# Kernel optimization log

Measured on AMD Instinct MI355X. Metric: run time of the kernel, lower is better.

Reference implementation:

```python
import jax, jax.numpy as jnp
import numpy as np

NUM_USERS, NUM_ITEMS, D = 100000, 200000, 128
B, LLEN, SLEN = 4096, 200, 50
NEG = -1e9


def setup_inputs() -> dict:
    key = jax.random.key(0)
    ks = jax.random.split(key, 10)
    w_range = float(np.sqrt(3.0 / D))
    return {
        "user_table": 0.01 * jax.random.normal(ks[0], (NUM_USERS, D), dtype=jnp.float32),
        "item_table": 0.01 * jax.random.normal(ks[1], (NUM_ITEMS, D), dtype=jnp.float32),
        "W1": jax.random.uniform(ks[2], (2 * D, 16), minval=-w_range, maxval=w_range, dtype=jnp.float32),
        "b1": jnp.zeros((16,), dtype=jnp.float32),
        "W2": jax.random.uniform(ks[3], (16, 1), minval=-w_range, maxval=w_range, dtype=jnp.float32),
        "b2": jnp.zeros((1,), dtype=jnp.float32),
        "user_inputs": jax.random.randint(ks[4], (B,), 0, NUM_USERS, dtype=jnp.int64) if jax.config.jax_enable_x64 else jax.random.randint(ks[4], (B,), 0, NUM_USERS, dtype=jnp.int32),
        "L_inputs": jax.random.randint(ks[5], (B, LLEN), 0, NUM_ITEMS, dtype=jnp.int32),
        "S_inputs": jax.random.randint(ks[6], (B, SLEN), 0, NUM_ITEMS, dtype=jnp.int32),
        "item_inputs": jax.random.randint(ks[7], (B,), 0, NUM_ITEMS, dtype=jnp.int32),
    }


def reference(user_table, item_table, W1, b1, W2, b2,
              user_inputs, L_inputs, S_inputs, item_inputs):
    def att_logits(x):  # x: [..., 2D] -> [...]
        h = jax.nn.relu(x @ W1 + b1)
        return (h @ W2 + b2)[..., 0]

    def masked_softmax(logits, mask):  # softmax over last axis restricted to mask
        logits = jnp.where(mask, logits, NEG)
        return jax.nn.softmax(logits, axis=-1)

    u_emb = user_table[user_inputs]                      # [B, D]

    # ---- long-term attention over L history ----
    L_mask = L_inputs >= 0                               # [B, L]
    L_idx = jnp.where(L_mask, L_inputs, 0)
    L_emb = item_table[L_idx]                            # [B, L, D]
    uL = jnp.concatenate([jnp.broadcast_to(u_emb[:, None, :], L_emb.shape), L_emb], axis=-1)  # [B, L, 2D]
    w1 = masked_softmax(att_logits(uL), L_mask)          # [B, L]
    u_long = jnp.einsum('bl,bld->bd', w1, L_emb)         # [B, D]

    # ---- short-term attention over [u_long] + S (L assumed nonempty) ----
    S_mask = S_inputs >= 0                               # [B, S]
    S_idx = jnp.where(S_mask, S_inputs, 0)
    S_emb = item_table[S_idx]                            # [B, S, D]
    seq = jnp.concatenate([u_long[:, None, :], S_emb], axis=1)   # [B, 1+S, D]
    seq_mask = jnp.concatenate([jnp.ones((seq.shape[0], 1), dtype=bool), S_mask], axis=1)
    uSeq = jnp.concatenate([jnp.broadcast_to(u_emb[:, None, :], seq.shape), seq], axis=-1)  # [B, 1+S, 2D]
    w2 = masked_softmax(att_logits(uSeq), seq_mask)      # [B, 1+S]
    user_hybrid = jnp.einsum('bs,bsd->bd', w2, seq)      # [B, D]

    # ---- score: bmm([B,1,D], [B,D,1]) -> [B,1,1] ----
    item_emb = item_table[item_inputs]                   # [B, D]
    score = jnp.sum(user_hybrid * item_emb, axis=-1)[:, None, None]
    return score
```

## Files before the change

kernel.cpp:

```cpp
#include <hip/hip_runtime.h>
#include <math.h>

#define D 128
#define LLEN 200
#define SLEN 50
#define CH 56
#define ESTR 132

__device__ __forceinline__ float wave_red_sum(float v) {
#pragma unroll
  for (int m = 32; m >= 1; m >>= 1) v += __shfl_xor(v, m, 64);
  return v;
}
__device__ __forceinline__ float block_sum(float v, float* red) {
  v = wave_red_sum(v);
  if ((threadIdx.x & 63) == 0) red[threadIdx.x >> 6] = v;
  __syncthreads();
  v = red[0] + red[1] + red[2] + red[3];
  __syncthreads();
  return v;
}

#define GATHER_L(dst, IT, BASE)                        \
  do {                                                 \
    int s_ = tid + (IT);                               \
    int gid_ = rows1[(BASE) + (s_ >> 5)];              \
    if (gid_ < 0) gid_ = 0;                            \
    dst = it4[(size_t)gid_ * 32 + (s_ & 31)];          \
  } while (0)

#define GATHER_S(dst, IT)                              \
  do {                                                 \
    int s_ = tid + (IT);                               \
    int gid_ = rowsS[s_ >> 5];                         \
    if (gid_ < 0) gid_ = 0;                            \
    dst = it4[(size_t)gid_ * 32 + (s_ & 31)];          \
  } while (0)

#define STORE_L(src, IT)                                                     \
  do {                                                                       \
    int s_ = tid + (IT);                                                     \
    reinterpret_cast<float4*>(&ebuf[(s_ >> 5) * ESTR])[s_ & 31] = src;       \
  } while (0)

#define STORE_S(src, IT)                                                     \
  do {                                                                       \
    int s_ = tid + (IT);                                                     \
    reinterpret_cast<float4*>(&ebuf[((s_ >> 5) + 1) * ESTR])[s_ & 31] = src; \
  } while (0)

#define FMA4(WL, P, ACC)                \
  do {                                  \
    ACC.x = fmaf((WL), P.x, ACC.x);     \
    ACC.y = fmaf((WL), P.y, ACC.y);     \
    ACC.z = fmaf((WL), P.z, ACC.z);     \
  } while (0);                          \
  ACC.w = fmaf((WL), P.w, ACC.w)

#define MATVEC_HS(CNT)                                                      \
  if (lane < (CNT)) {                                                       \
    float a0 = 0.f, a1 = 0.f, a2 = 0.f, a3 = 0.f;                           \
    const float4* er4 = reinterpret_cast<const float4*>(&ebuf[lane * ESTR]);\
    const float* wc = &W1[(size_t)D * 16 + 4 * w];                          \
    _Pragma("unroll 8")                                                     \
    for (int k = 0; k < 32; ++k) {                                          \
      float4 e = er4[k];                                                    \
      const float* wr = wc + k * 64;            \
      a0 = fmaf(e.x, wr[0],  a0); a1 = fmaf(e.x, wr[1],  a1);               \
      a2 = fmaf(e.x, wr[2],  a2); a3 = fmaf(e.x, wr[3],  a3);               \
      a0 = fmaf(e.y, wr[16], a0); a1 = fmaf(e.y, wr[17], a1);               \
      a2 = fmaf(e.y, wr[18], a2); a3 = fmaf(e.y, wr[19], a3);               \
      a0 = fmaf(e.z, wr[32], a0); a1 = fmaf(e.z, wr[33], a1);               \
      a2 = fmaf(e.z, wr[34], a2); a3 = fmaf(e.z, wr[35], a3);               \
      a0 = fmaf(e.w, wr[48], a0); a1 = fmaf(e.w, wr[49], a1);               \
      a2 = fmaf(e.w, wr[50], a2); a3 = fmaf(e.w, wr[51], a3);               \
    }                                                                       \
    float hs = fmaxf(upart_sh[4 * w + 0] + a0, 0.f) * w2a;                  \
    hs = fmaf(fmaxf(upart_sh[4 * w + 1] + a1, 0.f), w2b, hs);               \
    hs = fmaf(fmaxf(upart_sh[4 * w + 2] + a2, 0.f), w2c, hs);               \
    hs = fmaf(fmaxf(upart_sh[4 * w + 3] + a3, 0.f), w2d, hs);               \
    hspart[w * 65 + lane] = hs;                                             \
  }

#define FINALIZE_L(CNT, BASE)                                           \
  if (tid < (CNT)) {                                                    \
    float lg = hspart[tid] + hspart[65 + tid] + hspart[130 + tid] +     \
               hspart[195 + tid] + b2v;                                 \
    float p_ = (rows1[(BASE) + tid] >= 0) ? expf(lg) : 0.f;             \
    w_sh[tid] = p_;                                                     \
    pacc += p_;                                                         \
  }

__global__ void __launch_bounds__(256, 5) din_kernel(
    const float* __restrict__ user_table, const float* __restrict__ item_table,
    const float* __restrict__ W1, const float* __restrict__ b1,
    const float* __restrict__ W2, const float* __restrict__ b2,
    const int* __restrict__ user_inputs, const int* __restrict__ L_inputs,
    const int* __restrict__ S_inputs, const int* __restrict__ item_inputs,
    float* __restrict__ out) {
  __shared__ float ebuf[CH * ESTR];
  __shared__ float hspart[4 * 65];
  __shared__ float w_sh[CH];
  __shared__ int rows1[LLEN];
  __shared__ int rowsS[SLEN];
  __shared__ float upart_sh[16];
  __shared__ float red_sh[4];

  const int b = blockIdx.x;
  const int tid = threadIdx.x;
  const int lane = tid & 63;
  const int w = __builtin_amdgcn_readfirstlane(tid >> 6);
  const int col4 = tid & 31;
  const int grp = tid >> 5;
  const float4* it4 = reinterpret_cast<const float4*>(item_table);

  float* u_sh = &ebuf[0];
  float* part = &ebuf[128];
  if (tid < D) u_sh[tid] = user_table[(size_t)user_inputs[b] * D + tid];
  const float item_f =
      (tid < D) ? item_table[(size_t)item_inputs[b] * D + tid] : 0.f;
  if (tid < LLEN) rows1[tid] = L_inputs[(size_t)b * LLEN + tid];
  if (tid < SLEN) rowsS[tid] = S_inputs[(size_t)b * SLEN + tid];
  __syncthreads();

  float4 A0, A1, A2, A3, A4, A5, A6, B0, B1, B2, B3, B4, B5, B6;
  GATHER_L(A0, 0, 0);    GATHER_L(A1, 256, 0);  GATHER_L(A2, 512, 0);
  GATHER_L(A3, 768, 0);  GATHER_L(A4, 1024, 0); GATHER_L(A5, 1280, 0);
  GATHER_L(A6, 1536, 0);

  {
    int j = tid & 15, g = tid >> 4;
    float p = 0.f;
#pragma unroll
    for (int t = 0; t < 8; ++t) {
      int d = g * 8 + t;
      p = fmaf(u_sh[d], W1[d * 16 + j], p);
    }
    part[tid] = p;
  }
  __syncthreads();
  if (tid < 16) {
    float s = b1[tid];
#pragma unroll
    for (int g = 0; g < 16; ++g) s += part[g * 16 + tid];
    upart_sh[tid] = s;
  }
  __syncthreads();

  const float b2v = b2[0];
  const float w2a = W2[4 * w + 0], w2b = W2[4 * w + 1];
  const float w2c = W2[4 * w + 2], w2d = W2[4 * w + 3];

  float pacc = 0.f;
  float4 uacc = make_float4(0.f, 0.f, 0.f, 0.f);
  float wl;

  STORE_L(A0, 0);    STORE_L(A1, 256);  STORE_L(A2, 512);  STORE_L(A3, 768);
  STORE_L(A4, 1024); STORE_L(A5, 1280); STORE_L(A6, 1536);
  __syncthreads();
  MATVEC_HS(56);
  GATHER_L(B0, 0, 56);    GATHER_L(B1, 256, 56);  GATHER_L(B2, 512, 56);
  GATHER_L(B3, 768, 56);  GATHER_L(B4, 1024, 56); GATHER_L(B5, 1280, 56);
  GATHER_L(B6, 1536, 56);
  __syncthreads();
  FINALIZE_L(56, 0);
  __syncthreads();
  wl = w_sh[grp];      FMA4(wl, A0, uacc);
  wl = w_sh[grp + 8];  FMA4(wl, A1, uacc);
  wl = w_sh[grp + 16]; FMA4(wl, A2, uacc);
  wl = w_sh[grp + 24]; FMA4(wl, A3, uacc);
  wl = w_sh[grp + 32]; FMA4(wl, A4, uacc);
  wl = w_sh[grp + 40]; FMA4(wl, A5, uacc);
  wl = w_sh[grp + 48]; FMA4(wl, A6, uacc);

  STORE_L(B0, 0);    STORE_L(B1, 256);  STORE_L(B2, 512);  STORE_L(B3, 768);
  STORE_L(B4, 1024); STORE_L(B5, 1280); STORE_L(B6, 1536);
  __syncthreads();
  MATVEC_HS(56);
  GATHER_L(A0, 0, 112);    GATHER_L(A1, 256, 112);  GATHER_L(A2, 512, 112);
  GATHER_L(A3, 768, 112);  GATHER_L(A4, 1024, 112); GATHER_L(A5, 1280, 112);
  GATHER_L(A6, 1536, 112);
  __syncthreads();
  FINALIZE_L(56, 56);
  __syncthreads();
  wl = w_sh[grp];      FMA4(wl, B0, uacc);
  wl = w_sh[grp + 8];  FMA4(wl, B1, uacc);
  wl = w_sh[grp + 16]; FMA4(wl, B2, uacc);
  wl = w_sh[grp + 24]; FMA4(wl, B3, uacc);
  wl = w_sh[grp + 32]; FMA4(wl, B4, uacc);
  wl = w_sh[grp + 40]; FMA4(wl, B5, uacc);
  wl = w_sh[grp + 48]; FMA4(wl, B6, uacc);

  STORE_L(A0, 0);    STORE_L(A1, 256);  STORE_L(A2, 512);  STORE_L(A3, 768);
  STORE_L(A4, 1024); STORE_L(A5, 1280); STORE_L(A6, 1536);
  __syncthreads();
  MATVEC_HS(56);
  GATHER_L(B0, 0, 168); GATHER_L(B1, 256, 168);
  GATHER_L(B2, 512, 168); GATHER_L(B3, 768, 168);
  __syncthreads();
  FINALIZE_L(56, 112);
  __syncthreads();
  wl = w_sh[grp];      FMA4(wl, A0, uacc);
  wl = w_sh[grp + 8];  FMA4(wl, A1, uacc);
  wl = w_sh[grp + 16]; FMA4(wl, A2, uacc);
  wl = w_sh[grp + 24]; FMA4(wl, A3, uacc);
  wl = w_sh[grp + 32]; FMA4(wl, A4, uacc);
  wl = w_sh[grp + 40]; FMA4(wl, A5, uacc);
  wl = w_sh[grp + 48]; FMA4(wl, A6, uacc);

  STORE_L(B0, 0); STORE_L(B1, 256); STORE_L(B2, 512); STORE_L(B3, 768);
  __syncthreads();
  MATVEC_HS(32);
  GATHER_S(A0, 0);    GATHER_S(A1, 256);  GATHER_S(A2, 512);
  GATHER_S(A3, 768);  GATHER_S(A4, 1024); GATHER_S(A5, 1280);
  if (tid < 64) GATHER_S(A6, 1536);
  __syncthreads();
  FINALIZE_L(32, 168);
  __syncthreads();
  wl = w_sh[grp];      FMA4(wl, B0, uacc);
  wl = w_sh[grp + 8];  FMA4(wl, B1, uacc);
  wl = w_sh[grp + 16]; FMA4(wl, B2, uacc);
  wl = w_sh[grp + 24]; FMA4(wl, B3, uacc);

  const float invS1 = 1.f / block_sum(pacc, red_sh);
  uacc.x += __shfl_xor(uacc.x, 32, 64);
  uacc.y += __shfl_xor(uacc.y, 32, 64);
  uacc.z += __shfl_xor(uacc.z, 32, 64);
  uacc.w += __shfl_xor(uacc.w, 32, 64);
  float* scr = &ebuf[52 * ESTR];
  if (lane < 32) reinterpret_cast<float4*>(scr)[(w << 5) + lane] = uacc;
  STORE_S(A0, 0);    STORE_S(A1, 256);  STORE_S(A2, 512);
  STORE_S(A3, 768);  STORE_S(A4, 1024); STORE_S(A5, 1280);
  if (tid < 64) STORE_S(A6, 1536);
  __syncthreads();
  if (tid < D) {
    float s = scr[tid] + scr[128 + tid] + scr[256 + tid] + scr[384 + tid];
    ebuf[tid] = s * invS1;
  }
  __syncthreads();

  MATVEC_HS(51);
  __syncthreads();
  float pacc2 = 0.f;
  if (tid < 51) {
    float lg = hspart[tid] + hspart[65 + tid] + hspart[130 + tid] +
               hspart[195 + tid] + b2v;
    bool valid = (tid == 0) || (rowsS[tid - 1] >= 0);
    float p_ = valid ? expf(lg) : 0.f;
    w_sh[tid] = p_;
    pacc2 = p_;
  }
  __syncthreads();

  float4 uacc2 = make_float4(0.f, 0.f, 0.f, 0.f);
  if (grp == 0) {
    float wl0 = w_sh[0];
    const float4 e = reinterpret_cast<const float4*>(&ebuf[0])[col4];
    FMA4(wl0, e, uacc2);
  }
  wl = w_sh[1 + grp];      FMA4(wl, A0, uacc2);
  wl = w_sh[1 + grp + 8];  FMA4(wl, A1, uacc2);
  wl = w_sh[1 + grp + 16]; FMA4(wl, A2, uacc2);
  wl = w_sh[1 + grp + 24]; FMA4(wl, A3, uacc2);
  wl = w_sh[1 + grp + 32]; FMA4(wl, A4, uacc2);
  wl = w_sh[1 + grp + 40]; FMA4(wl, A5, uacc2);
  if (grp < 2) { wl = w_sh[1 + grp + 48]; FMA4(wl, A6, uacc2); }

  const float invS2 = 1.f / block_sum(pacc2, red_sh);
  uacc2.x += __shfl_xor(uacc2.x, 32, 64);
  uacc2.y += __shfl_xor(uacc2.y, 32, 64);
  uacc2.z += __shfl_xor(uacc2.z, 32, 64);
  uacc2.w += __shfl_xor(uacc2.w, 32, 64);
  if (lane < 32) reinterpret_cast<float4*>(scr)[(w << 5) + lane] = uacc2;
  __syncthreads();

  float sv = 0.f;
  if (tid < D) {
    float s = scr[tid] + scr[128 + tid] + scr[256 + tid] + scr[384 + tid];
    sv = s * invS2 * item_f;
  }
  float tot = block_sum(sv, red_sh);
  if (tid == 0) out[b] = tot;
}

extern "C" void kernel_launch(void* const* d_in, const int* in_sizes, int n_in,
                              void* d_out, int out_size, void* d_ws, size_t ws_size,
                              hipStream_t stream) {
  const float* user_table = (const float*)d_in[0];
  const float* item_table = (const float*)d_in[1];
  const float* W1 = (const float*)d_in[2];
  const float* b1 = (const float*)d_in[3];
  const float* W2 = (const float*)d_in[4];
  const float* b2 = (const float*)d_in[5];
  const int* user_inputs = (const int*)d_in[6];
  const int* L_inputs = (const int*)d_in[7];
  const int* S_inputs = (const int*)d_in[8];
  const int* item_inputs = (const int*)d_in[9];
  float* out = (float*)d_out;

  const int B = in_sizes[6];
  din_kernel<<<B, 256, 0, stream>>>(user_table, item_table, W1, b1, W2, b2,
                                    user_inputs, L_inputs, S_inputs, item_inputs,
                                    out);
}
```

Measured before the change: 256.5 us.

## Compute attention MLP logits with bf16 MFMA over 64-row chunks

Replaces the scalar fp32 per-row matvec against W1 with bf16 MFMA 16x16x32 instructions. Gathered item embeddings are converted to bf16 and staged in shared memory, and W1 fragments are preloaded into registers. The chunk size grows from 56 to 64 rows, and the short-sequence gather is overlapped with the last long chunk. This cuts VALU work and shared-memory traffic for the logit computation, at the cost of bf16 precision in the logits and lower occupancy (launch bounds 5 to 4).

```diff
diff --git a/kernel.cpp b/kernel.cpp
--- a/kernel.cpp
+++ b/kernel.cpp
@@ -4,8 +4,15 @@
 #define D 128
 #define LLEN 200
 #define SLEN 50
-#define CH 56
-#define ESTR 132
+#define TSTR 136
+
+typedef __attribute__((ext_vector_type(8))) short short8;
+typedef __attribute__((ext_vector_type(4))) float f32x4;
+
+__device__ __forceinline__ unsigned short f2bf(float f) {
+  unsigned int u = __float_as_uint(f);
+  return (unsigned short)((u + 0x7FFFu + ((u >> 16) & 1u)) >> 16);
+}
 
 __device__ __forceinline__ float wave_red_sum(float v) {
 #pragma unroll
@@ -37,16 +44,14 @@
     dst = it4[(size_t)gid_ * 32 + (s_ & 31)];          \
   } while (0)
 
-#define STORE_L(src, IT)                                                     \
-  do {                                                                       \
-    int s_ = tid + (IT);                                                     \
-    reinterpret_cast<float4*>(&ebuf[(s_ >> 5) * ESTR])[s_ & 31] = src;       \
-  } while (0)
-
-#define STORE_S(src, IT)                                                     \
-  do {                                                                       \
-    int s_ = tid + (IT);                                                     \
-    reinterpret_cast<float4*>(&ebuf[((s_ >> 5) + 1) * ESTR])[s_ & 31] = src; \
+#define STOREB(src, IT, RO)                                                   \
+  do {                                                                        \
+    int s_ = tid + (IT);                                                      \
+    ushort4 q_;                                                               \
+    q_.x = f2bf(src.x); q_.y = f2bf(src.y);                                   \
+    q_.z = f2bf(src.z); q_.w = f2bf(src.w);                                   \
+    *reinterpret_cast<ushort4*>(&tb[((s_ >> 5) + (RO)) * TSTR +               \
+                                    4 * (s_ & 31)]) = q_;                     \
   } while (0)
 
 #define FMA4(WL, P, ACC)                \
@@ -57,50 +62,66 @@
   } while (0);                          \
   ACC.w = fmaf((WL), P.w, ACC.w)
 
-#define MATVEC_HS(CNT)                                                      \
-  if (lane < (CNT)) {                                                       \
-    float a0 = 0.f, a1 = 0.f, a2 = 0.f, a3 = 0.f;                           \
-    const float4* er4 = reinterpret_cast<const float4*>(&ebuf[lane * ESTR]);\
-    const float* wc = &W1[(size_t)D * 16 + 4 * w];                          \
-    _Pragma("unroll 8")                                                     \
-    for (int k = 0; k < 32; ++k) {                                          \
-      float4 e = er4[k];                                                    \
-      const float* wr = wc + k * 64;            \
-      a0 = fmaf(e.x, wr[0],  a0); a1 = fmaf(e.x, wr[1],  a1);               \
-      a2 = fmaf(e.x, wr[2],  a2); a3 = fmaf(e.x, wr[3],  a3);               \
-      a0 = fmaf(e.y, wr[16], a0); a1 = fmaf(e.y, wr[17], a1);               \
-      a2 = fmaf(e.y, wr[18], a2); a3 = fmaf(e.y, wr[19], a3);               \
-      a0 = fmaf(e.z, wr[32], a0); a1 = fmaf(e.z, wr[33], a1);               \
-      a2 = fmaf(e.z, wr[34], a2); a3 = fmaf(e.z, wr[35], a3);               \
-      a0 = fmaf(e.w, wr[48], a0); a1 = fmaf(e.w, wr[49], a1);               \
-      a2 = fmaf(e.w, wr[50], a2); a3 = fmaf(e.w, wr[51], a3);               \
-    }                                                                       \
-    float hs = fmaxf(upart_sh[4 * w + 0] + a0, 0.f) * w2a;                  \
-    hs = fmaf(fmaxf(upart_sh[4 * w + 1] + a1, 0.f), w2b, hs);               \
-    hs = fmaf(fmaxf(upart_sh[4 * w + 2] + a2, 0.f), w2c, hs);               \
-    hs = fmaf(fmaxf(upart_sh[4 * w + 3] + a3, 0.f), w2d, hs);               \
-    hspart[w * 65 + lane] = hs;                                             \
-  }
-
-#define FINALIZE_L(CNT, BASE)                                           \
-  if (tid < (CNT)) {                                                    \
-    float lg = hspart[tid] + hspart[65 + tid] + hspart[130 + tid] +     \
-               hspart[195 + tid] + b2v;                                 \
-    float p_ = (rows1[(BASE) + tid] >= 0) ? expf(lg) : 0.f;             \
-    w_sh[tid] = p_;                                                     \
-    pacc += p_;                                                         \
-  }
-
-__global__ void __launch_bounds__(256, 5) din_kernel(
+template <int MODE>
+__device__ __forceinline__ void mfma_logits(
+    const unsigned short* tb, short8 Bf0, short8 Bf1, short8 Bf2, short8 Bf3,
+    int w, int lane, float upart_j, float w2j, float b2v,
+    const int* rowm, int nvalid, float* w_sh, float& pacc) {
+  const int row = 16 * w + (lane & 15);
+  const unsigned short* ap = &tb[row * TSTR + 8 * (lane >> 4)];
+  short8 a0 = *reinterpret_cast<const short8*>(ap);
+  short8 a1 = *reinterpret_cast<const short8*>(ap + 32);
+  short8 a2 = *reinterpret_cast<const short8*>(ap + 64);
+  short8 a3 = *reinterpret_cast<const short8*>(ap + 96);
+  f32x4 acc = {0.f, 0.f, 0.f, 0.f};
+  acc = __builtin_amdgcn_mfma_f32_16x16x32_bf16(a0, Bf0, acc, 0, 0, 0);
+  acc = __builtin_amdgcn_mfma_f32_16x16x32_bf16(a1, Bf1, acc, 0, 0, 0);
+  acc = __builtin_amdgcn_mfma_f32_16x16x32_bf16(a2, Bf2, acc, 0, 0, 0);
+  acc = __builtin_amdgcn_mfma_f32_16x16x32_bf16(a3, Bf3, acc, 0, 0, 0);
+  float v0 = fmaxf(upart_j + acc[0], 0.f) * w2j;
+  float v1 = fmaxf(upart_j + acc[1], 0.f) * w2j;
+  float v2 = fmaxf(upart_j + acc[2], 0.f) * w2j;
+  float v3 = fmaxf(upart_j + acc[3], 0.f) * w2j;
+#pragma unroll
+  for (int m = 1; m <= 8; m <<= 1) {
+    v0 += __shfl_xor(v0, m, 64);
+    v1 += __shfl_xor(v1, m, 64);
+    v2 += __shfl_xor(v2, m, 64);
+    v3 += __shfl_xor(v3, m, 64);
+  }
+  if ((lane & 15) == 0) {
+    const int it0 = 16 * w + 4 * (lane >> 4);
+    float p0, p1, p2, p3;
+    if (MODE == 0) {
+      p0 = (it0 + 0 < nvalid && rowm[it0 + 0] >= 0) ? expf(v0 + b2v) : 0.f;
+      p1 = (it0 + 1 < nvalid && rowm[it0 + 1] >= 0) ? expf(v1 + b2v) : 0.f;
+      p2 = (it0 + 2 < nvalid && rowm[it0 + 2] >= 0) ? expf(v2 + b2v) : 0.f;
+      p3 = (it0 + 3 < nvalid && rowm[it0 + 3] >= 0) ? expf(v3 + b2v) : 0.f;
+    } else {
+      p0 = (it0 == 0) ? expf(v0 + b2v)
+                      : ((it0 < nvalid && rowm[it0 - 1] >= 0) ? expf(v0 + b2v) : 0.f);
+      p1 = (it0 + 1 < nvalid && rowm[it0 + 0] >= 0) ? expf(v1 + b2v) : 0.f;
+      p2 = (it0 + 2 < nvalid && rowm[it0 + 1] >= 0) ? expf(v2 + b2v) : 0.f;
+      p3 = (it0 + 3 < nvalid && rowm[it0 + 2] >= 0) ? expf(v3 + b2v) : 0.f;
+    }
+    float4 pv;
+    pv.x = p0; pv.y = p1; pv.z = p2; pv.w = p3;
+    reinterpret_cast<float4*>(w_sh)[it0 >> 2] = pv;
+    pacc += p0 + p1 + p2 + p3;
+  }
+}
+
+__global__ void __launch_bounds__(256, 4) din_kernel(
     const float* __restrict__ user_table, const float* __restrict__ item_table,
     const float* __restrict__ W1, const float* __restrict__ b1,
     const float* __restrict__ W2, const float* __restrict__ b2,
     const int* __restrict__ user_inputs, const int* __restrict__ L_inputs,
     const int* __restrict__ S_inputs, const int* __restrict__ item_inputs,
     float* __restrict__ out) {
-  __shared__ float ebuf[CH * ESTR];
-  __shared__ float hspart[4 * 65];
-  __shared__ float w_sh[CH];
+  __shared__ __align__(16) unsigned short tb[64 * TSTR];
+  __shared__ __align__(16) float scratch[512];
+  __shared__ __align__(16) float ul_sh[128];
+  __shared__ __align__(16) float w_sh[64];
   __shared__ int rows1[LLEN];
   __shared__ int rowsS[SLEN];
   __shared__ float upart_sh[16];
@@ -114,8 +135,8 @@
   const int grp = tid >> 5;
   const float4* it4 = reinterpret_cast<const float4*>(item_table);
 
-  float* u_sh = &ebuf[0];
-  float* part = &ebuf[128];
+  float* u_sh = &scratch[0];
+  float* part = &scratch[128];
   if (tid < D) u_sh[tid] = user_table[(size_t)user_inputs[b] * D + tid];
   const float item_f =
       (tid < D) ? item_table[(size_t)item_inputs[b] * D + tid] : 0.f;
@@ -123,10 +144,23 @@
   if (tid < SLEN) rowsS[tid] = S_inputs[(size_t)b * SLEN + tid];
   __syncthreads();
 
-  float4 A0, A1, A2, A3, A4, A5, A6, B0, B1, B2, B3, B4, B5, B6;
+  float4 A0, A1, A2, A3, A4, A5, A6, A7, B0, B1, B2, B3, B4, B5, B6, B7;
   GATHER_L(A0, 0, 0);    GATHER_L(A1, 256, 0);  GATHER_L(A2, 512, 0);
   GATHER_L(A3, 768, 0);  GATHER_L(A4, 1024, 0); GATHER_L(A5, 1280, 0);
-  GATHER_L(A6, 1536, 0);
+  GATHER_L(A6, 1536, 0); GATHER_L(A7, 1792, 0);
+
+  short8 Bf0, Bf1, Bf2, Bf3;
+  {
+    const int j = lane & 15, ko = lane >> 4;
+    const float* wp = &W1[(size_t)(128 + 8 * ko) * 16 + j];
+#pragma unroll
+    for (int t = 0; t < 8; ++t) {
+      Bf0[t] = (short)f2bf(wp[t * 16]);
+      Bf1[t] = (short)f2bf(wp[(32 + t) * 16]);
+      Bf2[t] = (short)f2bf(wp[(64 + t) * 16]);
+      Bf3[t] = (short)f2bf(wp[(96 + t) * 16]);
+    }
+  }
 
   {
     int j = tid & 15, g = tid >> 4;
@@ -148,22 +182,22 @@
   __syncthreads();
 
   const float b2v = b2[0];
-  const float w2a = W2[4 * w + 0], w2b = W2[4 * w + 1];
-  const float w2c = W2[4 * w + 2], w2d = W2[4 * w + 3];
+  const float upart_j = upart_sh[lane & 15];
+  const float w2j = W2[lane & 15];
 
   float pacc = 0.f;
   float4 uacc = make_float4(0.f, 0.f, 0.f, 0.f);
   float wl;
 
-  STORE_L(A0, 0);    STORE_L(A1, 256);  STORE_L(A2, 512);  STORE_L(A3, 768);
-  STORE_L(A4, 1024); STORE_L(A5, 1280); STORE_L(A6, 1536);
-  __syncthreads();
-  MATVEC_HS(56);
-  GATHER_L(B0, 0, 56);    GATHER_L(B1, 256, 56);  GATHER_L(B2, 512, 56);
-  GATHER_L(B3, 768, 56);  GATHER_L(B4, 1024, 56); GATHER_L(B5, 1280, 56);
-  GATHER_L(B6, 1536, 56);
-  __syncthreads();
-  FINALIZE_L(56, 0);
+  STOREB(A0, 0, 0);    STOREB(A1, 256, 0);  STOREB(A2, 512, 0);
+  STOREB(A3, 768, 0);  STOREB(A4, 1024, 0); STOREB(A5, 1280, 0);
+  STOREB(A6, 1536, 0); STOREB(A7, 1792, 0);
+  GATHER_L(B0, 0, 64);    GATHER_L(B1, 256, 64);  GATHER_L(B2, 512, 64);
+  GATHER_L(B3, 768, 64);  GATHER_L(B4, 1024, 64); GATHER_L(B5, 1280, 64);
+  GATHER_L(B6, 1536, 64); GATHER_L(B7, 1792, 64);
+  __syncthreads();
+  mfma_logits<0>(tb, Bf0, Bf1, Bf2, Bf3, w, lane, upart_j, w2j, b2v,
+                 rows1 + 0, 64, w_sh, pacc);
   __syncthreads();
   wl = w_sh[grp];      FMA4(wl, A0, uacc);
   wl = w_sh[grp + 8];  FMA4(wl, A1, uacc);
@@ -172,16 +206,17 @@
   wl = w_sh[grp + 32]; FMA4(wl, A4, uacc);
   wl = w_sh[grp + 40]; FMA4(wl, A5, uacc);
   wl = w_sh[grp + 48]; FMA4(wl, A6, uacc);
-
-  STORE_L(B0, 0);    STORE_L(B1, 256);  STORE_L(B2, 512);  STORE_L(B3, 768);
-  STORE_L(B4, 1024); STORE_L(B5, 1280); STORE_L(B6, 1536);
-  __syncthreads();
-  MATVEC_HS(56);
-  GATHER_L(A0, 0, 112);    GATHER_L(A1, 256, 112);  GATHER_L(A2, 512, 112);
-  GATHER_L(A3, 768, 112);  GATHER_L(A4, 1024, 112); GATHER_L(A5, 1280, 112);
-  GATHER_L(A6, 1536, 112);
-  __syncthreads();
-  FINALIZE_L(56, 56);
+  wl = w_sh[grp + 56]; FMA4(wl, A7, uacc);
+
+  STOREB(B0, 0, 0);    STOREB(B1, 256, 0);  STOREB(B2, 512, 0);
+  STOREB(B3, 768, 0);  STOREB(B4, 1024, 0); STOREB(B5, 1280, 0);
+  STOREB(B6, 1536, 0); STOREB(B7, 1792, 0);
+  GATHER_L(A0, 0, 128);    GATHER_L(A1, 256, 128);  GATHER_L(A2, 512, 128);
+  GATHER_L(A3, 768, 128);  GATHER_L(A4, 1024, 128); GATHER_L(A5, 1280, 128);
+  GATHER_L(A6, 1536, 128); GATHER_L(A7, 1792, 128);
+  __syncthreads();
+  mfma_logits<0>(tb, Bf0, Bf1, Bf2, Bf3, w, lane, upart_j, w2j, b2v,
+                 rows1 + 64, 64, w_sh, pacc);
   __syncthreads();
   wl = w_sh[grp];      FMA4(wl, B0, uacc);
   wl = w_sh[grp + 8];  FMA4(wl, B1, uacc);
@@ -190,15 +225,18 @@
   wl = w_sh[grp + 32]; FMA4(wl, B4, uacc);
   wl = w_sh[grp + 40]; FMA4(wl, B5, uacc);
   wl = w_sh[grp + 48]; FMA4(wl, B6, uacc);
-
-  STORE_L(A0, 0);    STORE_L(A1, 256);  STORE_L(A2, 512);  STORE_L(A3, 768);
-  STORE_L(A4, 1024); STORE_L(A5, 1280); STORE_L(A6, 1536);
-  __syncthreads();
-  MATVEC_HS(56);
-  GATHER_L(B0, 0, 168); GATHER_L(B1, 256, 168);
-  GATHER_L(B2, 512, 168); GATHER_L(B3, 768, 168);
-  __syncthreads();
-  FINALIZE_L(56, 112);
+  wl = w_sh[grp + 56]; FMA4(wl, B7, uacc);
+
+  STOREB(A0, 0, 0);    STOREB(A1, 256, 0);  STOREB(A2, 512, 0);
+  STOREB(A3, 768, 0);  STOREB(A4, 1024, 0); STOREB(A5, 1280, 0);
+  STOREB(A6, 1536, 0); STOREB(A7, 1792, 0);
+  GATHER_L(B0, 0, 192);
+  GATHER_S(B1, 0);    GATHER_S(B2, 256);  GATHER_S(B3, 512);
+  GATHER_S(B4, 768);  GATHER_S(B5, 1024); GATHER_S(B6, 1280);
+  if (tid < 64) GATHER_S(B7, 1536);
+  __syncthreads();
+  mfma_logits<0>(tb, Bf0, Bf1, Bf2, Bf3, w, lane, upart_j, w2j, b2v,
+                 rows1 + 128, 64, w_sh, pacc);
   __syncthreads();
   wl = w_sh[grp];      FMA4(wl, A0, uacc);
   wl = w_sh[grp + 8];  FMA4(wl, A1, uacc);
@@ -207,76 +245,66 @@
   wl = w_sh[grp + 32]; FMA4(wl, A4, uacc);
   wl = w_sh[grp + 40]; FMA4(wl, A5, uacc);
   wl = w_sh[grp + 48]; FMA4(wl, A6, uacc);
-
-  STORE_L(B0, 0); STORE_L(B1, 256); STORE_L(B2, 512); STORE_L(B3, 768);
-  __syncthreads();
-  MATVEC_HS(32);
-  GATHER_S(A0, 0);    GATHER_S(A1, 256);  GATHER_S(A2, 512);
-  GATHER_S(A3, 768);  GATHER_S(A4, 1024); GATHER_S(A5, 1280);
-  if (tid < 64) GATHER_S(A6, 1536);
-  __syncthreads();
-  FINALIZE_L(32, 168);
-  __syncthreads();
-  wl = w_sh[grp];      FMA4(wl, B0, uacc);
-  wl = w_sh[grp + 8];  FMA4(wl, B1, uacc);
-  wl = w_sh[grp + 16]; FMA4(wl, B2, uacc);
-  wl = w_sh[grp + 24]; FMA4(wl, B3, uacc);
+  wl = w_sh[grp + 56]; FMA4(wl, A7, uacc);
+
+  STOREB(B0, 0, 0);
+  __syncthreads();
+  if (w == 0)
+    mfma_logits<0>(tb, Bf0, Bf1, Bf2, Bf3, w, lane, upart_j, w2j, b2v,
+                   rows1 + 192, 8, w_sh, pacc);
+  __syncthreads();
+  wl = w_sh[grp];
+  FMA4(wl, B0, uacc);
 
   const float invS1 = 1.f / block_sum(pacc, red_sh);
   uacc.x += __shfl_xor(uacc.x, 32, 64);
   uacc.y += __shfl_xor(uacc.y, 32, 64);
   uacc.z += __shfl_xor(uacc.z, 32, 64);
   uacc.w += __shfl_xor(uacc.w, 32, 64);
-  float* scr = &ebuf[52 * ESTR];
-  if (lane < 32) reinterpret_cast<float4*>(scr)[(w << 5) + lane] = uacc;
-  STORE_S(A0, 0);    STORE_S(A1, 256);  STORE_S(A2, 512);
-  STORE_S(A3, 768);  STORE_S(A4, 1024); STORE_S(A5, 1280);
-  if (tid < 64) STORE_S(A6, 1536);
+  if (lane < 32) reinterpret_cast<float4*>(scratch)[(w << 5) + lane] = uacc;
+  STOREB(B1, 0, 1);    STOREB(B2, 256, 1);  STOREB(B3, 512, 1);
+  STOREB(B4, 768, 1);  STOREB(B5, 1024, 1); STOREB(B6, 1280, 1);
+  if (tid < 64) STOREB(B7, 1536, 1);
   __syncthreads();
   if (tid < D) {
-    float s = scr[tid] + scr[128 + tid] + scr[256 + tid] + scr[384 + tid];
-    ebuf[tid] = s * invS1;
-  }
-  __syncthreads();
-
-  MATVEC_HS(51);
-  __syncthreads();
+    float s = scratch[tid] + scratch[128 + tid] + scratch[256 + tid] +
+              scratch[384 + tid];
+    float ul = s * invS1;
+    ul_sh[tid] = ul;
+    tb[tid] = f2bf(ul);
+  }
+  __syncthreads();
+
   float pacc2 = 0.f;
-  if (tid < 51) {
-    float lg = hspart[tid] + hspart[65 + tid] + hspart[130 + tid] +
-               hspart[195 + tid] + b2v;
-    bool valid = (tid == 0) || (rowsS[tid - 1] >= 0);
-    float p_ = valid ? expf(lg) : 0.f;
-    w_sh[tid] = p_;
-    pacc2 = p_;
-  }
-  __syncthreads();
+  mfma_logits<1>(tb, Bf0, Bf1, Bf2, Bf3, w, lane, upart_j, w2j, b2v,
+                 rowsS, 51, w_sh, pacc2);
+  const float invS2 = 1.f / block_sum(pacc2, red_sh);
 
   float4 uacc2 = make_float4(0.f, 0.f, 0.f, 0.f);
   if (grp == 0) {
     float wl0 = w_sh[0];
-    const float4 e = reinterpret_cast<const float4*>(&ebuf[0])[col4];
+    const float4 e = reinterpret_cast<const float4*>(ul_sh)[col4];
     FMA4(wl0, e, uacc2);
   }
-  wl = w_sh[1 + grp];      FMA4(wl, A0, uacc2);
-  wl = w_sh[1 + grp + 8];  FMA4(wl, A1, uacc2);
-  wl = w_sh[1 + grp + 16]; FMA4(wl, A2, uacc2);
-  wl = w_sh[1 + grp + 24]; FMA4(wl, A3, uacc2);
-  wl = w_sh[1 + grp + 32]; FMA4(wl, A4, uacc2);
-  wl = w_sh[1 + grp + 40]; FMA4(wl, A5, uacc2);
-  if (grp < 2) { wl = w_sh[1 + grp + 48]; FMA4(wl, A6, uacc2); }
-
-  const float invS2 = 1.f / block_sum(pacc2, red_sh);
+  wl = w_sh[1 + grp];  FMA4(wl, B1, uacc2);
+  wl = w_sh[9 + grp];  FMA4(wl, B2, uacc2);
+  wl = w_sh[17 + grp]; FMA4(wl, B3, uacc2);
+  wl = w_sh[25 + grp]; FMA4(wl, B4, uacc2);
+  wl = w_sh[33 + grp]; FMA4(wl, B5, uacc2);
+  wl = w_sh[41 + grp]; FMA4(wl, B6, uacc2);
+  if (grp < 2) { wl = w_sh[49 + grp]; FMA4(wl, B7, uacc2); }
+
   uacc2.x += __shfl_xor(uacc2.x, 32, 64);
   uacc2.y += __shfl_xor(uacc2.y, 32, 64);
   uacc2.z += __shfl_xor(uacc2.z, 32, 64);
   uacc2.w += __shfl_xor(uacc2.w, 32, 64);
-  if (lane < 32) reinterpret_cast<float4*>(scr)[(w << 5) + lane] = uacc2;
+  if (lane < 32) reinterpret_cast<float4*>(scratch)[(w << 5) + lane] = uacc2;
   __syncthreads();
 
   float sv = 0.f;
   if (tid < D) {
-    float s = scr[tid] + scr[128 + tid] + scr[256 + tid] + scr[384 + tid];
+    float s = scratch[tid] + scratch[128 + tid] + scratch[256 + tid] +
+              scratch[384 + tid];
     sv = s * invS2 * item_f;
   }
   float tot = block_sum(sv, red_sh);
```

Result: slower. 297.5 us (+16.0%).
